# Optimization experiments

Hardware: AMD Instinct MI355X
Metric: run time of the kernel (lower is better)

## Reference

```python
import jax, jax.numpy as jnp
import numpy as np

LOG_STD2 = float(np.log(0.001))  # matches nn.init posterior_W_u/v fill, unused: params are random here


def _mvg_layer(x, M, u, v, eps):
    # append ones column (bias trick): [B, in] -> [B, in+1]
    x1 = jnp.concatenate([x, jnp.ones((x.shape[0], 1), x.dtype)], axis=1)
    # W = M + diag(exp(.5u)) @ eps @ diag(exp(.5v))  ==  M + row/col scaled eps
    W = M + jnp.exp(0.5 * u)[:, None] * eps * jnp.exp(0.5 * v)[None, :]
    return x1 @ W


def setup_inputs() -> dict:
    key = jax.random.key(0)
    ks = jax.random.split(key, 17)
    dims = [(2049, 4096), (4097, 4096), (4097, 4096), (4097, 2048)]
    inp = {"x": jax.random.normal(ks[0], (8192, 2048), dtype=jnp.float32)}
    ki = 1
    for i, (fin, fout) in enumerate(dims):
        inp[f"M{i}"] = jax.random.normal(ks[ki], (fin, fout), dtype=jnp.float32) * 0.001; ki += 1
        inp[f"u{i}"] = jax.random.normal(ks[ki], (fin,), dtype=jnp.float32) + LOG_STD2; ki += 1
        inp[f"v{i}"] = jax.random.normal(ks[ki], (fout,), dtype=jnp.float32) + LOG_STD2; ki += 1
        inp[f"eps{i}"] = jax.random.normal(ks[ki], (fin, fout), dtype=jnp.float32); ki += 1
    return inp


def reference(x, M0, u0, v0, eps0, M1, u1, v1, eps1, M2, u2, v2, eps2, M3, u3, v3, eps3):
    h = _mvg_layer(x, M0, u0, v0, eps0)
    h = _mvg_layer(jax.nn.relu(h), M1, u1, v1, eps1)
    h = _mvg_layer(jax.nn.relu(h), M2, u2, v2, eps2)
    h = _mvg_layer(jax.nn.relu(h), M3, u3, v3, eps3)
    return h
```

## Files before the change

### kernel.cpp

```cpp
#include <hip/hip_runtime.h>
#include <cstdint>
#include <cstddef>

typedef __bf16 bf16_t;
typedef __attribute__((ext_vector_type(8))) __bf16 bf16x8;
typedef __attribute__((ext_vector_type(4))) __bf16 bf16x4;
typedef __attribute__((ext_vector_type(4))) float floatx4;

__device__ __forceinline__ void cp16(const void* g, void* l) {
  __builtin_amdgcn_global_load_lds(
      (const __attribute__((address_space(1))) void*)(uintptr_t)g,
      (__attribute__((address_space(3))) void*)(uintptr_t)l, 16, 0, 0);
}

__device__ __forceinline__ void stage_half(const bf16_t* p, int K, char* dst,
                                           int tid) {
  cp16(p, dst + tid * 16);
  cp16(p + (size_t)128 * K, dst + 8192 + tid * 16);
}

__global__ void cvt_to_bf16(const float4* __restrict__ in,
                            bf16x4* __restrict__ out, int n4) {
  int i = blockIdx.x * 256 + threadIdx.x;
  if (i < n4) {
    float4 f = in[i];
    bf16x4 o;
    o[0] = (bf16_t)f.x; o[1] = (bf16_t)f.y; o[2] = (bf16_t)f.z; o[3] = (bf16_t)f.w;
    out[i] = o;
  }
}

__global__ void prep_wt(const float* __restrict__ M, const float* __restrict__ u,
                        const float* __restrict__ v, const float* __restrict__ eps,
                        bf16_t* __restrict__ Wt, int K, int N) {
  __shared__ float tile[32][33];
  const int nb = blockIdx.x * 32, kb = blockIdx.y * 32;
  const int tx = threadIdx.x, ty = threadIdx.y;
  const float sv = __expf(0.5f * v[nb + tx]);
#pragma unroll
  for (int r = 0; r < 4; ++r) {
    const int k = kb + ty + 8 * r;
    const float su = __expf(0.5f * u[k]);
    const size_t idx = (size_t)k * N + nb + tx;
    tile[ty + 8 * r][tx] = M[idx] + su * eps[idx] * sv;
  }
  __syncthreads();
#pragma unroll
  for (int r = 0; r < 4; ++r) {
    const int n = nb + ty + 8 * r;
    Wt[(size_t)n * K + kb + tx] = (bf16_t)tile[tx][ty + 8 * r];
  }
}

__global__ void prep_bias(const float* __restrict__ M, const float* __restrict__ u,
                          const float* __restrict__ v, const float* __restrict__ eps,
                          float* __restrict__ bias, int K, int N) {
  int n = blockIdx.x * 256 + threadIdx.x;
  if (n < N) {
    const size_t idx = (size_t)K * N + n;
    bias[n] = M[idx] + __expf(0.5f * u[K]) * eps[idx] * __expf(0.5f * v[n]);
  }
}

template <int CURB>
__device__ __forceinline__ void ktile(int t, int NT, int K,
                                      const bf16_t* gA, const bf16_t* gB,
                                      char* lds, int tid, int aoff0, int boff0,
                                      floatx4 (&acc)[8][4]) {
  constexpr int curO = CURB * 65536;
  constexpr int nxtO = (CURB ^ 1) * 65536;
  bf16x8 af[4], bb[4];

#pragma unroll
  for (int m = 0; m < 4; ++m)
    af[m] = *(const bf16x8*)(lds + curO + aoff0 + m * 1024);
#pragma unroll
  for (int n = 0; n < 4; ++n)
    bb[n] = *(const bf16x8*)(lds + curO + 32768 + boff0 + n * 1024);
  if (t + 1 < NT)
    stage_half(gA + (size_t)(t + 1) * 64 + 32, K, lds + nxtO + 16384, tid);
  __builtin_amdgcn_s_barrier();
  asm volatile("s_waitcnt lgkmcnt(0)" ::: "memory");
  __builtin_amdgcn_sched_barrier(0);
  __builtin_amdgcn_s_setprio(1);
#pragma unroll
  for (int m = 0; m < 4; ++m)
#pragma unroll
    for (int n = 0; n < 4; ++n)
      acc[m][n] = __builtin_amdgcn_mfma_f32_16x16x32_bf16(af[m], bb[n],
                                                          acc[m][n], 0, 0, 0);
  __builtin_amdgcn_s_setprio(0);
  __builtin_amdgcn_sched_barrier(0);
  __builtin_amdgcn_s_barrier();

#pragma unroll
  for (int m = 0; m < 4; ++m)
    af[m] = *(const bf16x8*)(lds + curO + aoff0 + (m + 4) * 1024);
  if (t + 1 < NT)
    stage_half(gB + (size_t)(t + 1) * 64 + 32, K, lds + nxtO + 49152, tid);
  __builtin_amdgcn_s_barrier();
  asm volatile("s_waitcnt lgkmcnt(0)" ::: "memory");
  __builtin_amdgcn_sched_barrier(0);
  __builtin_amdgcn_s_setprio(1);
#pragma unroll
  for (int m = 0; m < 4; ++m)
#pragma unroll
    for (int n = 0; n < 4; ++n)
      acc[m + 4][n] = __builtin_amdgcn_mfma_f32_16x16x32_bf16(af[m], bb[n],
                                                              acc[m + 4][n], 0, 0, 0);
  __builtin_amdgcn_s_setprio(0);
  __builtin_amdgcn_sched_barrier(0);
  __builtin_amdgcn_s_barrier();

#pragma unroll
  for (int m = 0; m < 4; ++m)
    af[m] = *(const bf16x8*)(lds + curO + 16384 + aoff0 + m * 1024);
#pragma unroll
  for (int n = 0; n < 4; ++n)
    bb[n] = *(const bf16x8*)(lds + curO + 49152 + boff0 + n * 1024);
  if (t + 2 < NT)
    stage_half(gA + (size_t)(t + 2) * 64, K, lds + curO, tid);
  __builtin_amdgcn_s_barrier();
  asm volatile("s_waitcnt lgkmcnt(0)" ::: "memory");
  __builtin_amdgcn_sched_barrier(0);
  __builtin_amdgcn_s_setprio(1);
#pragma unroll
  for (int m = 0; m < 4; ++m)
#pragma unroll
    for (int n = 0; n < 4; ++n)
      acc[m][n] = __builtin_amdgcn_mfma_f32_16x16x32_bf16(af[m], bb[n],
                                                          acc[m][n], 0, 0, 0);
  __builtin_amdgcn_s_setprio(0);
  __builtin_amdgcn_sched_barrier(0);
  __builtin_amdgcn_s_barrier();

#pragma unroll
  for (int m = 0; m < 4; ++m)
    af[m] = *(const bf16x8*)(lds + curO + 16384 + aoff0 + (m + 4) * 1024);
  if (t + 2 < NT)
    stage_half(gB + (size_t)(t + 2) * 64, K, lds + curO + 32768, tid);
  __builtin_amdgcn_s_barrier();
  asm volatile("s_waitcnt lgkmcnt(0)" ::: "memory");
  __builtin_amdgcn_sched_barrier(0);
  __builtin_amdgcn_s_setprio(1);
#pragma unroll
  for (int m = 0; m < 4; ++m)
#pragma unroll
    for (int n = 0; n < 4; ++n)
      acc[m + 4][n] = __builtin_amdgcn_mfma_f32_16x16x32_bf16(af[m], bb[n],
                                                              acc[m + 4][n], 0, 0, 0);
  __builtin_amdgcn_s_setprio(0);
  __builtin_amdgcn_sched_barrier(0);
  if (t + 2 < NT) {
    asm volatile("s_waitcnt vmcnt(4)" ::: "memory");
  } else if (t + 1 < NT) {
    asm volatile("s_waitcnt vmcnt(0)" ::: "memory");
  }
  __builtin_amdgcn_s_barrier();
}

template <int EPI>
__global__ __launch_bounds__(512, 2) void gemm256(
    const bf16_t* __restrict__ A, const bf16_t* __restrict__ Bt,
    const float* __restrict__ bias, void* __restrict__ Cout, int N, int K) {
  extern __shared__ char lds[];
  const int tid = threadIdx.x;
  const int lane = tid & 63;
  const int wave = tid >> 6;
  const int wm = (wave >> 2) * 128;
  const int wn = (wave & 3) * 64;
  const int l15 = lane & 15;
  const int kqs = ((lane >> 4) ^ ((lane >> 1) & 3)) << 4;
  const int aoff0 = (wm + l15) * 64 + kqs;
  const int bofB0 = (wn + l15) * 64 + kqs;

  const int gx = gridDim.x;
  int id = blockIdx.y * gx + blockIdx.x;
  const int cpx = (gx * (int)gridDim.y) >> 3;
  id = (id & 7) * cpx + (id >> 3);
  const int bm = (id / gx) * 256;
  const int bn = (id % gx) * 256;

  const int srow = tid >> 2;
  const int ss8 = ((tid & 3) ^ ((tid >> 3) & 3)) * 8;
  const bf16_t* gA = A + (size_t)(bm + srow) * K + ss8;
  const bf16_t* gB = Bt + (size_t)(bn + srow) * K + ss8;

  const int NT = K >> 6;

  floatx4 acc[8][4] = {};

  stage_half(gA, K, lds + 0, tid);
  stage_half(gA + 32, K, lds + 16384, tid);
  stage_half(gB, K, lds + 32768, tid);
  stage_half(gB + 32, K, lds + 49152, tid);
  stage_half(gA + 64, K, lds + 65536, tid);
  stage_half(gB + 64, K, lds + 65536 + 32768, tid);
  asm volatile("s_waitcnt vmcnt(4)" ::: "memory");
  __builtin_amdgcn_s_barrier();

  for (int t = 0; t < NT; t += 2) {
    ktile<0>(t, NT, K, gA, gB, lds, tid, aoff0, bofB0, acc);
    ktile<1>(t + 1, NT, K, gA, gB, lds, tid, aoff0, bofB0, acc);
  }

  const int kq4 = lane >> 4;
  const int col0 = bn + wn + l15;
  const int row0 = bm + wm + kq4 * 4;
#pragma unroll
  for (int j = 0; j < 4; ++j) {
    const float bj = bias[col0 + j * 16];
#pragma unroll
    for (int m = 0; m < 8; ++m) {
#pragma unroll
      for (int r = 0; r < 4; ++r) {
        float v = acc[m][j][r] + bj;
        const size_t idx = (size_t)(row0 + m * 16 + r) * N + (col0 + j * 16);
        if (EPI == 0) {
          v = v > 0.f ? v : 0.f;
          ((bf16_t*)Cout)[idx] = (bf16_t)v;
        } else {
          ((float*)Cout)[idx] = v;
        }
      }
    }
  }
}

extern "C" void kernel_launch(void* const* d_in, const int* in_sizes, int n_in,
                              void* d_out, int out_size, void* d_ws, size_t ws_size,
                              hipStream_t stream) {
  const float* x = (const float*)d_in[0];
  const float *Mm[4], *uu[4], *vv[4], *ee[4];
  for (int i = 0; i < 4; ++i) {
    Mm[i] = (const float*)d_in[1 + 4 * i];
    uu[i] = (const float*)d_in[2 + 4 * i];
    vv[i] = (const float*)d_in[3 + 4 * i];
    ee[i] = (const float*)d_in[4 + 4 * i];
  }

  char* ws = (char*)d_ws;
  bf16_t* Wt0 = (bf16_t*)ws;
  bf16_t* Wt1 = (bf16_t*)(ws + 16777216);
  bf16_t* Wt2 = (bf16_t*)(ws + 16777216 + 33554432);
  bf16_t* Wt3 = (bf16_t*)(ws + 16777216 + 2u * 33554432);
  char* bptr = ws + 2u * 16777216 + 2u * 33554432;
  float* bias0 = (float*)(bptr);
  float* bias1 = (float*)(bptr + 16384);
  float* bias2 = (float*)(bptr + 32768);
  float* bias3 = (float*)(bptr + 49152);
  char* act = bptr + 65536;
  bf16_t* hA = (bf16_t*)act;
  bf16_t* hB = (bf16_t*)(act + 67108864);
  bf16_t* xb = (bf16_t*)d_out;

  static bool attr_set = false;
  if (!attr_set) {
    (void)hipFuncSetAttribute(reinterpret_cast<const void*>(&gemm256<0>),
                              hipFuncAttributeMaxDynamicSharedMemorySize, 131072);
    (void)hipFuncSetAttribute(reinterpret_cast<const void*>(&gemm256<1>),
                              hipFuncAttributeMaxDynamicSharedMemorySize, 131072);
    attr_set = true;
  }

  cvt_to_bf16<<<16384, 256, 0, stream>>>((const float4*)x, (bf16x4*)xb,
                                         8192 * 2048 / 4);
  prep_wt<<<dim3(4096 / 32, 2048 / 32), dim3(32, 8), 0, stream>>>(
      Mm[0], uu[0], vv[0], ee[0], Wt0, 2048, 4096);
  prep_wt<<<dim3(4096 / 32, 4096 / 32), dim3(32, 8), 0, stream>>>(
      Mm[1], uu[1], vv[1], ee[1], Wt1, 4096, 4096);
  prep_wt<<<dim3(4096 / 32, 4096 / 32), dim3(32, 8), 0, stream>>>(
      Mm[2], uu[2], vv[2], ee[2], Wt2, 4096, 4096);
  prep_wt<<<dim3(2048 / 32, 4096 / 32), dim3(32, 8), 0, stream>>>(
      Mm[3], uu[3], vv[3], ee[3], Wt3, 4096, 2048);
  prep_bias<<<16, 256, 0, stream>>>(Mm[0], uu[0], vv[0], ee[0], bias0, 2048, 4096);
  prep_bias<<<16, 256, 0, stream>>>(Mm[1], uu[1], vv[1], ee[1], bias1, 4096, 4096);
  prep_bias<<<16, 256, 0, stream>>>(Mm[2], uu[2], vv[2], ee[2], bias2, 4096, 4096);
  prep_bias<<<8, 256, 0, stream>>>(Mm[3], uu[3], vv[3], ee[3], bias3, 4096, 2048);

  gemm256<0><<<dim3(16, 32), 512, 131072, stream>>>(xb, Wt0, bias0, hA, 4096, 2048);
  gemm256<0><<<dim3(16, 32), 512, 131072, stream>>>(hA, Wt1, bias1, hB, 4096, 4096);
  gemm256<0><<<dim3(16, 32), 512, 131072, stream>>>(hB, Wt2, bias2, hA, 4096, 4096);
  gemm256<1><<<dim3(8, 32), 512, 131072, stream>>>(hA, Wt3, bias3, d_out, 2048, 4096);
}
```

Before: 1.171 ms.

## Interleave LDS reads with MFMAs via staggered lgkmcnt waits and vectorize epilogue

Restructures each k-tile phase so A fragments are loaded one at a time and MFMAs begin as soon as each load lands, using graded lgkmcnt waits instead of a full wait. One barrier per phase is removed. MFMA operand order is swapped to produce a transposed accumulator layout, which lets the epilogue use vectorized bias loads and 4-wide stores. The four bias-prep launches are merged into one. Removing barriers and the finer scheduling risk LDS hazards or compiler reordering issues.

```diff
diff --git a/kernel.cpp b/kernel.cpp
--- a/kernel.cpp
+++ b/kernel.cpp
@@ -6,6 +6,13 @@
 typedef __attribute__((ext_vector_type(8))) __bf16 bf16x8;
 typedef __attribute__((ext_vector_type(4))) __bf16 bf16x4;
 typedef __attribute__((ext_vector_type(4))) float floatx4;
+
+#define SB0 __builtin_amdgcn_sched_barrier(0)
+#define LGKM(N)                                          \
+  do {                                                   \
+    asm volatile("s_waitcnt lgkmcnt(" #N ")" ::: "memory"); \
+    SB0;                                                 \
+  } while (0)
 
 __device__ __forceinline__ void cp16(const void* g, void* l) {
   __builtin_amdgcn_global_load_lds(
@@ -52,14 +59,86 @@
   }
 }
 
-__global__ void prep_bias(const float* __restrict__ M, const float* __restrict__ u,
-                          const float* __restrict__ v, const float* __restrict__ eps,
-                          float* __restrict__ bias, int K, int N) {
-  int n = blockIdx.x * 256 + threadIdx.x;
+struct BiasArgs {
+  const float* M[4];
+  const float* u[4];
+  const float* v[4];
+  const float* e[4];
+  float* b[4];
+};
+__global__ void prep_bias_all(BiasArgs a) {
+  const int bid = blockIdx.x;
+  int layer, base;
+  if (bid < 16) { layer = 0; base = bid; }
+  else if (bid < 32) { layer = 1; base = bid - 16; }
+  else if (bid < 48) { layer = 2; base = bid - 32; }
+  else { layer = 3; base = bid - 48; }
+  const int K = (layer == 0) ? 2048 : 4096;
+  const int N = (layer == 3) ? 2048 : 4096;
+  const int n = base * 256 + threadIdx.x;
   if (n < N) {
     const size_t idx = (size_t)K * N + n;
-    bias[n] = M[idx] + __expf(0.5f * u[K]) * eps[idx] * __expf(0.5f * v[n]);
-  }
+    a.b[layer][n] = a.M[layer][idx] +
+                    __expf(0.5f * a.u[layer][K]) * a.e[layer][idx] *
+                        __expf(0.5f * a.v[layer][n]);
+  }
+}
+
+template <int I0>
+__device__ __forceinline__ void mfma_quad(const bf16x8 (&bb)[4], bf16x8 a,
+                                          floatx4 (&acc)[8][4]) {
+#pragma unroll
+  for (int j = 0; j < 4; ++j)
+    acc[I0][j] =
+        __builtin_amdgcn_mfma_f32_16x16x32_bf16(bb[j], a, acc[I0][j], 0, 0, 0);
+}
+
+template <int I0>
+__device__ __forceinline__ void phaseA(const char* Ab, const char* Bb,
+                                       bf16x8 (&bb)[4], floatx4 (&acc)[8][4]) {
+  bf16x8 af0 = *(const bf16x8*)(Ab + (I0 + 0) * 1024);
+  bb[0] = *(const bf16x8*)(Bb);
+  bb[1] = *(const bf16x8*)(Bb + 1024);
+  bb[2] = *(const bf16x8*)(Bb + 2048);
+  bb[3] = *(const bf16x8*)(Bb + 3072);
+  SB0;
+  bf16x8 af1 = *(const bf16x8*)(Ab + (I0 + 1) * 1024);
+  SB0;
+  bf16x8 af2 = *(const bf16x8*)(Ab + (I0 + 2) * 1024);
+  SB0;
+  bf16x8 af3 = *(const bf16x8*)(Ab + (I0 + 3) * 1024);
+  __builtin_amdgcn_s_setprio(1);
+  LGKM(3);
+  mfma_quad<I0 + 0>(bb, af0, acc);
+  LGKM(2);
+  mfma_quad<I0 + 1>(bb, af1, acc);
+  LGKM(1);
+  mfma_quad<I0 + 2>(bb, af2, acc);
+  LGKM(0);
+  mfma_quad<I0 + 3>(bb, af3, acc);
+  __builtin_amdgcn_s_setprio(0);
+}
+
+template <int I0>
+__device__ __forceinline__ void phaseB(const char* Ab, const bf16x8 (&bb)[4],
+                                       floatx4 (&acc)[8][4]) {
+  bf16x8 af0 = *(const bf16x8*)(Ab + (I0 + 0) * 1024);
+  SB0;
+  bf16x8 af1 = *(const bf16x8*)(Ab + (I0 + 1) * 1024);
+  SB0;
+  bf16x8 af2 = *(const bf16x8*)(Ab + (I0 + 2) * 1024);
+  SB0;
+  bf16x8 af3 = *(const bf16x8*)(Ab + (I0 + 3) * 1024);
+  __builtin_amdgcn_s_setprio(1);
+  LGKM(3);
+  mfma_quad<I0 + 0>(bb, af0, acc);
+  LGKM(2);
+  mfma_quad<I0 + 1>(bb, af1, acc);
+  LGKM(1);
+  mfma_quad<I0 + 2>(bb, af2, acc);
+  LGKM(0);
+  mfma_quad<I0 + 3>(bb, af3, acc);
+  __builtin_amdgcn_s_setprio(0);
 }
 
 template <int CURB>
@@ -69,94 +148,41 @@
                                       floatx4 (&acc)[8][4]) {
   constexpr int curO = CURB * 65536;
   constexpr int nxtO = (CURB ^ 1) * 65536;
-  bf16x8 af[4], bb[4];
-
-#pragma unroll
-  for (int m = 0; m < 4; ++m)
-    af[m] = *(const bf16x8*)(lds + curO + aoff0 + m * 1024);
-#pragma unroll
-  for (int n = 0; n < 4; ++n)
-    bb[n] = *(const bf16x8*)(lds + curO + 32768 + boff0 + n * 1024);
+  bf16x8 bb[4];
+  const char* Ab0 = lds + curO + aoff0;
+  const char* Ab1 = lds + curO + 16384 + aoff0;
+  const char* Bb0 = lds + curO + 32768 + boff0;
+  const char* Bb1 = lds + curO + 49152 + boff0;
+
   if (t + 1 < NT)
     stage_half(gA + (size_t)(t + 1) * 64 + 32, K, lds + nxtO + 16384, tid);
-  __builtin_amdgcn_s_barrier();
-  asm volatile("s_waitcnt lgkmcnt(0)" ::: "memory");
-  __builtin_amdgcn_sched_barrier(0);
-  __builtin_amdgcn_s_setprio(1);
-#pragma unroll
-  for (int m = 0; m < 4; ++m)
-#pragma unroll
-    for (int n = 0; n < 4; ++n)
-      acc[m][n] = __builtin_amdgcn_mfma_f32_16x16x32_bf16(af[m], bb[n],
-                                                          acc[m][n], 0, 0, 0);
-  __builtin_amdgcn_s_setprio(0);
-  __builtin_amdgcn_sched_barrier(0);
-  __builtin_amdgcn_s_barrier();
-
-#pragma unroll
-  for (int m = 0; m < 4; ++m)
-    af[m] = *(const bf16x8*)(lds + curO + aoff0 + (m + 4) * 1024);
+  phaseA<0>(Ab0, Bb0, bb, acc);
+  __builtin_amdgcn_s_barrier();
+  SB0;
+
   if (t + 1 < NT)
     stage_half(gB + (size_t)(t + 1) * 64 + 32, K, lds + nxtO + 49152, tid);
-  __builtin_amdgcn_s_barrier();
-  asm volatile("s_waitcnt lgkmcnt(0)" ::: "memory");
-  __builtin_amdgcn_sched_barrier(0);
-  __builtin_amdgcn_s_setprio(1);
-#pragma unroll
-  for (int m = 0; m < 4; ++m)
-#pragma unroll
-    for (int n = 0; n < 4; ++n)
-      acc[m + 4][n] = __builtin_amdgcn_mfma_f32_16x16x32_bf16(af[m], bb[n],
-                                                              acc[m + 4][n], 0, 0, 0);
-  __builtin_amdgcn_s_setprio(0);
-  __builtin_amdgcn_sched_barrier(0);
-  __builtin_amdgcn_s_barrier();
-
-#pragma unroll
-  for (int m = 0; m < 4; ++m)
-    af[m] = *(const bf16x8*)(lds + curO + 16384 + aoff0 + m * 1024);
-#pragma unroll
-  for (int n = 0; n < 4; ++n)
-    bb[n] = *(const bf16x8*)(lds + curO + 49152 + boff0 + n * 1024);
+  phaseB<4>(Ab0, bb, acc);
+  __builtin_amdgcn_s_barrier();
+  SB0;
+
   if (t + 2 < NT)
     stage_half(gA + (size_t)(t + 2) * 64, K, lds + curO, tid);
-  __builtin_amdgcn_s_barrier();
-  asm volatile("s_waitcnt lgkmcnt(0)" ::: "memory");
-  __builtin_amdgcn_sched_barrier(0);
-  __builtin_amdgcn_s_setprio(1);
-#pragma unroll
-  for (int m = 0; m < 4; ++m)
-#pragma unroll
-    for (int n = 0; n < 4; ++n)
-      acc[m][n] = __builtin_amdgcn_mfma_f32_16x16x32_bf16(af[m], bb[n],
-                                                          acc[m][n], 0, 0, 0);
-  __builtin_amdgcn_s_setprio(0);
-  __builtin_amdgcn_sched_barrier(0);
-  __builtin_amdgcn_s_barrier();
-
-#pragma unroll
-  for (int m = 0; m < 4; ++m)
-    af[m] = *(const bf16x8*)(lds + curO + 16384 + aoff0 + (m + 4) * 1024);
+  phaseA<0>(Ab1, Bb1, bb, acc);
+  __builtin_amdgcn_s_barrier();
+  SB0;
+
   if (t + 2 < NT)
     stage_half(gB + (size_t)(t + 2) * 64, K, lds + curO + 32768, tid);
-  __builtin_amdgcn_s_barrier();
-  asm volatile("s_waitcnt lgkmcnt(0)" ::: "memory");
-  __builtin_amdgcn_sched_barrier(0);
-  __builtin_amdgcn_s_setprio(1);
-#pragma unroll
-  for (int m = 0; m < 4; ++m)
-#pragma unroll
-    for (int n = 0; n < 4; ++n)
-      acc[m + 4][n] = __builtin_amdgcn_mfma_f32_16x16x32_bf16(af[m], bb[n],
-                                                              acc[m + 4][n], 0, 0, 0);
-  __builtin_amdgcn_s_setprio(0);
-  __builtin_amdgcn_sched_barrier(0);
+  phaseB<4>(Ab1, bb, acc);
   if (t + 2 < NT) {
     asm volatile("s_waitcnt vmcnt(4)" ::: "memory");
   } else if (t + 1 < NT) {
     asm volatile("s_waitcnt vmcnt(0)" ::: "memory");
   }
-  __builtin_amdgcn_s_barrier();
+  SB0;
+  __builtin_amdgcn_s_barrier();
+  SB0;
 }
 
 template <int EPI>
@@ -198,6 +224,7 @@
   stage_half(gB + 64, K, lds + 65536 + 32768, tid);
   asm volatile("s_waitcnt vmcnt(4)" ::: "memory");
   __builtin_amdgcn_s_barrier();
+  SB0;
 
   for (int t = 0; t < NT; t += 2) {
     ktile<0>(t, NT, K, gA, gB, lds, tid, aoff0, bofB0, acc);
@@ -205,23 +232,31 @@
   }
 
   const int kq4 = lane >> 4;
-  const int col0 = bn + wn + l15;
-  const int row0 = bm + wm + kq4 * 4;
-#pragma unroll
-  for (int j = 0; j < 4; ++j) {
-    const float bj = bias[col0 + j * 16];
-#pragma unroll
-    for (int m = 0; m < 8; ++m) {
-#pragma unroll
-      for (int r = 0; r < 4; ++r) {
-        float v = acc[m][j][r] + bj;
-        const size_t idx = (size_t)(row0 + m * 16 + r) * N + (col0 + j * 16);
-        if (EPI == 0) {
-          v = v > 0.f ? v : 0.f;
-          ((bf16_t*)Cout)[idx] = (bf16_t)v;
-        } else {
-          ((float*)Cout)[idx] = v;
-        }
+  const int row00 = bm + wm + l15;
+  const int colq = bn + wn + kq4 * 4;
+  float4 b4[4];
+#pragma unroll
+  for (int j = 0; j < 4; ++j) b4[j] = *(const float4*)&bias[colq + j * 16];
+#pragma unroll
+  for (int i = 0; i < 8; ++i) {
+    const size_t rbase = (size_t)(row00 + i * 16) * N;
+#pragma unroll
+    for (int j = 0; j < 4; ++j) {
+      float x0 = acc[i][j][0] + b4[j].x;
+      float x1 = acc[i][j][1] + b4[j].y;
+      float x2 = acc[i][j][2] + b4[j].z;
+      float x3 = acc[i][j][3] + b4[j].w;
+      if (EPI == 0) {
+        x0 = fmaxf(x0, 0.f);
+        x1 = fmaxf(x1, 0.f);
+        x2 = fmaxf(x2, 0.f);
+        x3 = fmaxf(x3, 0.f);
+        bf16x4 o;
+        o[0] = (bf16_t)x0; o[1] = (bf16_t)x1; o[2] = (bf16_t)x2; o[3] = (bf16_t)x3;
+        *(bf16x4*)((bf16_t*)Cout + rbase + colq + j * 16) = o;
+      } else {
+        float4 o = make_float4(x0, x1, x2, x3);
+        *(float4*)((float*)Cout + rbase + colq + j * 16) = o;
       }
     }
   }
@@ -273,10 +308,12 @@
       Mm[2], uu[2], vv[2], ee[2], Wt2, 4096, 4096);
   prep_wt<<<dim3(2048 / 32, 4096 / 32), dim3(32, 8), 0, stream>>>(
       Mm[3], uu[3], vv[3], ee[3], Wt3, 4096, 2048);
-  prep_bias<<<16, 256, 0, stream>>>(Mm[0], uu[0], vv[0], ee[0], bias0, 2048, 4096);
-  prep_bias<<<16, 256, 0, stream>>>(Mm[1], uu[1], vv[1], ee[1], bias1, 4096, 4096);
-  prep_bias<<<16, 256, 0, stream>>>(Mm[2], uu[2], vv[2], ee[2], bias2, 4096, 4096);
-  prep_bias<<<8, 256, 0, stream>>>(Mm[3], uu[3], vv[3], ee[3], bias3, 4096, 2048);
+  BiasArgs ba;
+  for (int i = 0; i < 4; ++i) {
+    ba.M[i] = Mm[i]; ba.u[i] = uu[i]; ba.v[i] = vv[i]; ba.e[i] = ee[i];
+  }
+  ba.b[0] = bias0; ba.b[1] = bias1; ba.b[2] = bias2; ba.b[3] = bias3;
+  prep_bias_all<<<56, 256, 0, stream>>>(ba);
 
   gemm256<0><<<dim3(16, 32), 512, 131072, stream>>>(xb, Wt0, bias0, hA, 4096, 2048);
   gemm256<0><<<dim3(16, 32), 512, 131072, stream>>>(hA, Wt1, bias1, hB, 4096, 4096);
```

Result: no change. 1.169 ms (-0.1%).
